# Optimization experiments

Hardware: AMD Instinct MI355X
Metric: run time of the kernel (lower is better)

The kernel has to match this reference:

```python
import jax, jax.numpy as jnp
import numpy as np
import math

E = 4096  # embed_dim
H = 32    # num_heads
M = 256   # max_queries
B = 8     # batch
N = 256   # kv tokens (16x16 grid -> no pos-embed interpolation branch)


def _sincos_1d(d, pos):
    omega = np.arange(d // 2, dtype=np.float32) / (d / 2.0)
    omega = 1.0 / 10000 ** omega
    out = np.einsum('m,d->md', pos.reshape(-1), omega)
    return np.concatenate([np.sin(out), np.cos(out)], axis=1)


def _sincos_2d(embed_dim, grid_size):
    gh = np.arange(grid_size, dtype=np.float32)
    gw = np.arange(grid_size, dtype=np.float32)
    grid = np.stack(np.meshgrid(gw, gh), axis=0).reshape(2, -1)
    return np.concatenate([
        _sincos_1d(embed_dim // 2, grid[0]),
        _sincos_1d(embed_dim // 2, grid[1]),
    ], axis=1)


def setup_inputs() -> dict:
    key = jax.random.key(0)
    ks = jax.random.split(key, 4)
    grid_size = int(math.ceil(math.sqrt(M)))
    pe = _sincos_2d(E, grid_size)[:M].astype(np.float32)
    return {
        'x': jax.random.normal(ks[0], (B, N, E), jnp.float32),
        'query': 0.02 * jax.random.normal(ks[1], (M, E), jnp.float32),
        'pos_embed': jnp.asarray(pe),
        'ln_q_w': jnp.ones((E,), jnp.float32),
        'ln_q_b': jnp.zeros((E,), jnp.float32),
        'ln_kv_w': jnp.ones((E,), jnp.float32),
        'ln_kv_b': jnp.zeros((E,), jnp.float32),
        'in_proj_w': 0.02 * jax.random.normal(ks[2], (3 * E, E), jnp.float32),
        'in_proj_b': jnp.zeros((3 * E,), jnp.float32),
        'out_proj_w': 0.02 * jax.random.normal(ks[3], (E, E), jnp.float32),
        'out_proj_b': jnp.zeros((E,), jnp.float32),
    }


def _ln(x, w, b, eps=1e-5):
    m = jnp.mean(x, -1, keepdims=True)
    v = jnp.mean((x - m) ** 2, -1, keepdims=True)
    return (x - m) * jax.lax.rsqrt(v + eps) * w + b


def reference(x, query, pos_embed, ln_q_w, ln_q_b, ln_kv_w, ln_kv_b,
              in_proj_w, in_proj_b, out_proj_w, out_proj_b):
    D = E // H
    kv = _ln(x, ln_kv_w, ln_kv_b)                      # [B,N,E] (kv_proj is Identity)
    q_in = _ln(query, ln_q_w, ln_q_b) + pos_embed      # [M,E] (Q + posQ, shared over batch)
    k_in = kv + pos_embed[None]                        # N == M so posK == pos_embed (no interp)
    Wq, Wk, Wv = in_proj_w[:E], in_proj_w[E:2 * E], in_proj_w[2 * E:]
    bq, bk, bv = in_proj_b[:E], in_proj_b[E:2 * E], in_proj_b[2 * E:]
    q = (q_in @ Wq.T + bq).reshape(M, H, D).transpose(1, 0, 2)          # [H,M,D]
    k = (k_in @ Wk.T + bk).reshape(B, N, H, D).transpose(0, 2, 1, 3)    # [B,H,N,D]
    v = (kv @ Wv.T + bv).reshape(B, N, H, D).transpose(0, 2, 1, 3)      # [B,H,N,D]
    scores = jnp.einsum('hmd,bhnd->bhmn', q, k) / jnp.sqrt(jnp.float32(D))
    attn = jax.nn.softmax(scores, axis=-1)                              # [B,H,M,N]
    o = jnp.einsum('bhmn,bhnd->bhmd', attn, v)
    o = o.transpose(0, 2, 1, 3).reshape(B, M, E)
    out = o @ out_proj_w.T + out_proj_b                                 # [B,M,E]
    # need_weights=True with average_attn_weights=True -> head-averaged weights
    return out, attn.mean(axis=1)
```

## Files before the change

kernel.cpp:

```cpp
#include <hip/hip_runtime.h>
#include <hip/hip_bf16.h>

typedef __bf16 bf16;
typedef __attribute__((ext_vector_type(8))) __bf16 bf16x8;
typedef __attribute__((ext_vector_type(4))) __bf16 bf16x4;
typedef __attribute__((ext_vector_type(4))) float floatx4;

#define E_DIM 4096
#define H_DIM 32
#define D_DIM 128
#define M_DIM 256
#define B_DIM 8
#define N_DIM 256

#define GLD_LDS(g, l) __builtin_amdgcn_global_load_lds( \
    (const __attribute__((address_space(1))) unsigned int*)(g), \
    (__attribute__((address_space(3))) unsigned int*)(l), 16, 0, 0)

__device__ __forceinline__ float wave_sum(float v) {
#pragma unroll
  for (int o = 32; o; o >>= 1) v += __shfl_xor(v, o);
  return v;
}
__device__ __forceinline__ float wave_max(float v) {
#pragma unroll
  for (int o = 32; o; o >>= 1) v = fmaxf(v, __shfl_xor(v, o));
  return v;
}

__global__ __launch_bounds__(256) void cvt_all_kernel(const float* __restrict__ s1,
                                                      bf16* __restrict__ d1,
                                                      const float* __restrict__ s2,
                                                      bf16* __restrict__ d2) {
  long i = ((long)blockIdx.x * 256 + threadIdx.x) * 8;
  const float* src;
  bf16* dst;
  if (i < 50331648L) { src = s1 + i; dst = d1 + i; }
  else { src = s2 + (i - 50331648L); dst = d2 + (i - 50331648L); }
  float4 a = *(const float4*)(src);
  float4 b = *(const float4*)(src + 4);
  bf16x8 p;
  p[0] = (bf16)a.x; p[1] = (bf16)a.y; p[2] = (bf16)a.z; p[3] = (bf16)a.w;
  p[4] = (bf16)b.x; p[5] = (bf16)b.y; p[6] = (bf16)b.z; p[7] = (bf16)b.w;
  *(bf16x8*)(dst) = p;
}

__global__ __launch_bounds__(256) void ln_x_kernel(const float* __restrict__ x,
                                                   const float* __restrict__ w,
                                                   const float* __restrict__ bvec,
                                                   const float* __restrict__ pos,
                                                   bf16* __restrict__ kv,
                                                   bf16* __restrict__ kin) {
  const int row = blockIdx.x;
  const int n = row & (N_DIM - 1);
  const int tid = threadIdx.x, wid = tid >> 6, lane = tid & 63;
  const float* xr = x + (size_t)row * E_DIM;
  float4 v[4];
  float s1 = 0.f, s2 = 0.f;
#pragma unroll
  for (int j = 0; j < 4; ++j) {
    v[j] = *(const float4*)(xr + j * 1024 + tid * 4);
    s1 += v[j].x + v[j].y + v[j].z + v[j].w;
    s2 += v[j].x * v[j].x + v[j].y * v[j].y + v[j].z * v[j].z + v[j].w * v[j].w;
  }
  s1 = wave_sum(s1); s2 = wave_sum(s2);
  __shared__ float red[8];
  if (lane == 0) { red[wid] = s1; red[wid + 4] = s2; }
  __syncthreads();
  s1 = red[0] + red[1] + red[2] + red[3];
  s2 = red[4] + red[5] + red[6] + red[7];
  const float mean = s1 * (1.f / E_DIM);
  const float var = s2 * (1.f / E_DIM) - mean * mean;
  const float rs = rsqrtf(var + 1e-5f);
#pragma unroll
  for (int j = 0; j < 4; ++j) {
    const int idx = j * 1024 + tid * 4;
    float4 wv = *(const float4*)(w + idx);
    float4 bv = *(const float4*)(bvec + idx);
    float4 pv = *(const float4*)(pos + (size_t)n * E_DIM + idx);
    float y0 = (v[j].x - mean) * rs * wv.x + bv.x;
    float y1 = (v[j].y - mean) * rs * wv.y + bv.y;
    float y2 = (v[j].z - mean) * rs * wv.z + bv.z;
    float y3 = (v[j].w - mean) * rs * wv.w + bv.w;
    bf16x4 a; a[0] = (bf16)y0; a[1] = (bf16)y1; a[2] = (bf16)y2; a[3] = (bf16)y3;
    *(bf16x4*)(kv + (size_t)row * E_DIM + idx) = a;
    bf16x4 c; c[0] = (bf16)(y0 + pv.x); c[1] = (bf16)(y1 + pv.y);
    c[2] = (bf16)(y2 + pv.z); c[3] = (bf16)(y3 + pv.w);
    *(bf16x4*)(kin + (size_t)row * E_DIM + idx) = c;
  }
}

__global__ __launch_bounds__(256) void ln_q_kernel(const float* __restrict__ q,
                                                   const float* __restrict__ w,
                                                   const float* __restrict__ bvec,
                                                   const float* __restrict__ pos,
                                                   bf16* __restrict__ qin) {
  const int row = blockIdx.x;
  const int tid = threadIdx.x, wid = tid >> 6, lane = tid & 63;
  const float* xr = q + (size_t)row * E_DIM;
  float4 v[4];
  float s1 = 0.f, s2 = 0.f;
#pragma unroll
  for (int j = 0; j < 4; ++j) {
    v[j] = *(const float4*)(xr + j * 1024 + tid * 4);
    s1 += v[j].x + v[j].y + v[j].z + v[j].w;
    s2 += v[j].x * v[j].x + v[j].y * v[j].y + v[j].z * v[j].z + v[j].w * v[j].w;
  }
  s1 = wave_sum(s1); s2 = wave_sum(s2);
  __shared__ float red[8];
  if (lane == 0) { red[wid] = s1; red[wid + 4] = s2; }
  __syncthreads();
  s1 = red[0] + red[1] + red[2] + red[3];
  s2 = red[4] + red[5] + red[6] + red[7];
  const float mean = s1 * (1.f / E_DIM);
  const float var = s2 * (1.f / E_DIM) - mean * mean;
  const float rs = rsqrtf(var + 1e-5f);
#pragma unroll
  for (int j = 0; j < 4; ++j) {
    const int idx = j * 1024 + tid * 4;
    float4 wv = *(const float4*)(w + idx);
    float4 bv = *(const float4*)(bvec + idx);
    float4 pv = *(const float4*)(pos + (size_t)row * E_DIM + idx);
    bf16x4 a;
    a[0] = (bf16)((v[j].x - mean) * rs * wv.x + bv.x + pv.x);
    a[1] = (bf16)((v[j].y - mean) * rs * wv.y + bv.y + pv.y);
    a[2] = (bf16)((v[j].z - mean) * rs * wv.z + bv.z + pv.z);
    a[3] = (bf16)((v[j].w - mean) * rs * wv.w + bv.w + pv.w);
    *(bf16x4*)(qin + (size_t)row * E_DIM + idx) = a;
  }
}

__global__ __launch_bounds__(256, 4)
void proj_fused(const bf16* __restrict__ qin, const bf16* __restrict__ kin,
                const bf16* __restrict__ kv, const bf16* __restrict__ Wqkv,
                const float* __restrict__ bqkv, bf16* __restrict__ qp,
                bf16* __restrict__ kp, bf16* __restrict__ vt) {
  __shared__ __align__(16) bf16 As[4096];
  __shared__ __align__(16) bf16 Bs[4096];
  const int tid = threadIdx.x;
  const int wid = tid >> 6;
  const int lane = tid & 63;

  const int id = blockIdx.x;
  int role, bx, by;
  const bf16 *A, *B;
  const float* bias;
  bf16* C;
  if (id < 512) {
    role = 1; bx = id & 31; by = id >> 5;
    A = kin; B = Wqkv + 16777216; bias = bqkv + 4096; C = kp;
  } else if (id < 1024) {
    role = 2; bx = (id - 512) & 31; by = (id - 512) >> 5;
    A = kv; B = Wqkv + 33554432; bias = bqkv + 8192; C = vt;
  } else {
    role = 0; bx = (id - 1024) & 31; by = (id - 1024) >> 5;
    A = qin; B = Wqkv; bias = bqkv; C = qp;
  }

  const bf16* Arow = A + (size_t)(by * 128) * E_DIM;
  const bf16* Brow = B + (size_t)(bx * 128) * E_DIM;

  const int s0 = wid * 2;
  const int srow = lane >> 2;
  const int skoff = (lane & 3) * 8;

  floatx4 acc[4][4];
#pragma unroll
  for (int i = 0; i < 4; ++i)
#pragma unroll
    for (int j = 0; j < 4; ++j) acc[i][j] = (floatx4){0.f, 0.f, 0.f, 0.f};

  const int rA = (wid >> 1) * 64 + (lane & 15);
  const int rB = (wid & 1) * 64 + (lane & 15);
  const int q16 = (lane >> 4) * 8;

  for (int kt = 0; kt < 128; ++kt) {
    const int k0 = kt << 5;
#pragma unroll
    for (int c = 0; c < 2; ++c) {
      const int s = s0 + c;
      const int row = s * 16 + srow;
      GLD_LDS(Arow + (size_t)row * E_DIM + k0 + skoff, As + s * 512);
      GLD_LDS(Brow + (size_t)row * E_DIM + k0 + skoff, Bs + s * 512);
    }
    asm volatile("s_waitcnt vmcnt(0)" ::: "memory");
    __syncthreads();

    bf16x8 af[4], bfr[4];
#pragma unroll
    for (int t = 0; t < 4; ++t) {
      af[t] = *(const bf16x8*)(As + (rA + t * 16) * 32 + q16);
      bfr[t] = *(const bf16x8*)(Bs + (rB + t * 16) * 32 + q16);
    }
#pragma unroll
    for (int tr = 0; tr < 4; ++tr)
#pragma unroll
      for (int tc = 0; tc < 4; ++tc)
        acc[tr][tc] = __builtin_amdgcn_mfma_f32_16x16x32_bf16(af[tr], bfr[tc],
                                                              acc[tr][tc], 0, 0, 0);
    __syncthreads();
  }

  const int mb = by * 128 + (wid >> 1) * 64 + (lane >> 4) * 4;
  const int nb = bx * 128 + (wid & 1) * 64 + (lane & 15);
#pragma unroll
  for (int tr = 0; tr < 4; ++tr) {
#pragma unroll
    for (int tc = 0; tc < 4; ++tc) {
      const int row0 = mb + tr * 16;
      const int col = nb + tc * 16;
      const float bb = bias[col];
      floatx4 a = acc[tr][tc];
      if (role != 2) {
#pragma unroll
        for (int r = 0; r < 4; ++r)
          C[(size_t)(row0 + r) * E_DIM + col] = (bf16)(a[r] + bb);
      } else {
        const int h = col >> 7, d = col & 127;
        const int b_ = row0 >> 8, n_ = row0 & 255;
        bf16x4 p;
#pragma unroll
        for (int r = 0; r < 4; ++r) p[r] = (bf16)(a[r] + bb);
        *(bf16x4*)(C + ((size_t)((b_ * H_DIM + h) * D_DIM + d)) * N_DIM + n_) = p;
      }
    }
  }
}

template <int MODE>
__global__ __launch_bounds__(256, 4)
void gemm_bt(const bf16* __restrict__ Abase, const bf16* __restrict__ Bbase,
             float* __restrict__ Cf, bf16* __restrict__ Cb,
             int K, int lda, int ldb, int ldc, float scale) {
  __shared__ __align__(16) bf16 As[4096];
  __shared__ __align__(16) bf16 Bs[4096];
  const int tid = threadIdx.x;
  const int wid = tid >> 6;
  const int lane = tid & 63;

  const bf16* A = Abase;
  const bf16* B = Bbase;
  int zb = 0, zh = 0;
  if constexpr (MODE == 2) {
    int z = blockIdx.z; zb = z >> 5; zh = z & 31;
    A += zh * D_DIM;
    B += ((size_t)zb * N_DIM) * E_DIM + zh * D_DIM;
  } else if constexpr (MODE == 3) {
    int z = blockIdx.z; zb = z >> 5; zh = z & 31;
    A += (size_t)z * M_DIM * 512;
    B += (size_t)z * D_DIM * N_DIM;
  } else if constexpr (MODE == 5) {
    A += blockIdx.z * 2048;
    B += blockIdx.z * 2048;
  }

  const bf16* Arow = A + (size_t)(blockIdx.y * 128) * lda;
  const bf16* Brow = B + (size_t)(blockIdx.x * 128) * ldb;

  const int s0 = wid * 2;
  const int srow = lane >> 2;
  const int skoff = (lane & 3) * 8;

  floatx4 acc[4][4];
#pragma unroll
  for (int i = 0; i < 4; ++i)
#pragma unroll
    for (int j = 0; j < 4; ++j) acc[i][j] = (floatx4){0.f, 0.f, 0.f, 0.f};

  const int rA = (wid >> 1) * 64 + (lane & 15);
  const int rB = (wid & 1) * 64 + (lane & 15);
  const int q16 = (lane >> 4) * 8;

  const int kTiles = K >> 5;
  for (int kt = 0; kt < kTiles; ++kt) {
    const int k0 = kt << 5;
#pragma unroll
    for (int c = 0; c < 2; ++c) {
      const int s = s0 + c;
      const int row = s * 16 + srow;
      GLD_LDS(Arow + (size_t)row * lda + k0 + skoff, As + s * 512);
      GLD_LDS(Brow + (size_t)row * ldb + k0 + skoff, Bs + s * 512);
    }
    asm volatile("s_waitcnt vmcnt(0)" ::: "memory");
    __syncthreads();

    bf16x8 af[4], bfr[4];
#pragma unroll
    for (int t = 0; t < 4; ++t) {
      af[t] = *(const bf16x8*)(As + (rA + t * 16) * 32 + q16);
      bfr[t] = *(const bf16x8*)(Bs + (rB + t * 16) * 32 + q16);
    }
#pragma unroll
    for (int tr = 0; tr < 4; ++tr)
#pragma unroll
      for (int tc = 0; tc < 4; ++tc)
        acc[tr][tc] = __builtin_amdgcn_mfma_f32_16x16x32_bf16(af[tr], bfr[tc],
                                                              acc[tr][tc], 0, 0, 0);
    __syncthreads();
  }

  const int mb = blockIdx.y * 128 + (wid >> 1) * 64 + (lane >> 4) * 4;
  const int nb = blockIdx.x * 128 + (wid & 1) * 64 + (lane & 15);
#pragma unroll
  for (int tr = 0; tr < 4; ++tr) {
#pragma unroll
    for (int tc = 0; tc < 4; ++tc) {
      const int row0 = mb + tr * 16;
      const int col = nb + tc * 16;
      floatx4 a = acc[tr][tc];
      if constexpr (MODE == 2) {
#pragma unroll
        for (int r = 0; r < 4; ++r)
          Cf[(size_t)blockIdx.z * (M_DIM * N_DIM) + (size_t)(row0 + r) * ldc + col] =
              a[r] * scale;
      } else if constexpr (MODE == 3) {
        int z = blockIdx.z; int zb_ = z >> 5, zh_ = z & 31;
#pragma unroll
        for (int r = 0; r < 4; ++r)
          Cb[(size_t)zb_ * M_DIM * E_DIM + (size_t)(row0 + r) * E_DIM + zh_ * D_DIM + col] =
              (bf16)a[r];
      } else {
#pragma unroll
        for (int r = 0; r < 4; ++r)
          Cf[(size_t)blockIdx.z * 8388608 + (size_t)(row0 + r) * ldc + col] = a[r];
      }
    }
  }
}

__global__ __launch_bounds__(256) void reduce_out_kernel(const float* __restrict__ p,
                                                         const float* __restrict__ bias,
                                                         float* __restrict__ out) {
  const size_t i = ((size_t)blockIdx.x * 256 + threadIdx.x) * 4;
  float4 a = *(const float4*)(p + i);
  float4 b = *(const float4*)(p + 8388608 + i);
  float4 bb = *(const float4*)(bias + (i & 4095));
  float4 o;
  o.x = a.x + b.x + bb.x; o.y = a.y + b.y + bb.y;
  o.z = a.z + b.z + bb.z; o.w = a.w + b.w + bb.w;
  *(float4*)(out + i) = o;
}

__global__ __launch_bounds__(256) void softmax_mean_kernel(float* __restrict__ scores,
                                                           float* __restrict__ out_mean) {
  const int bm = blockIdx.x;
  const int b = bm >> 8, m = bm & 255;
  const int wid = threadIdx.x >> 6, lane = threadIdx.x & 63;
  float a0 = 0.f, a1 = 0.f, a2 = 0.f, a3 = 0.f;
  for (int j = 0; j < 8; ++j) {
    const int h = wid * 8 + j;
    float* row = scores + ((size_t)((b * H_DIM + h) * M_DIM + m)) * N_DIM;
    float4 v = *(const float4*)(row + lane * 4);
    float mx = fmaxf(fmaxf(v.x, v.y), fmaxf(v.z, v.w));
    mx = wave_max(mx);
    v.x = __expf(v.x - mx); v.y = __expf(v.y - mx);
    v.z = __expf(v.z - mx); v.w = __expf(v.w - mx);
    const float s = wave_sum(v.x + v.y + v.z + v.w);
    const float inv = 1.f / s;
    v.x *= inv; v.y *= inv; v.z *= inv; v.w *= inv;
    a0 += v.x; a1 += v.y; a2 += v.z; a3 += v.w;
    bf16x4 p; p[0] = (bf16)v.x; p[1] = (bf16)v.y; p[2] = (bf16)v.z; p[3] = (bf16)v.w;
    *(bf16x4*)((bf16*)row + lane * 4) = p;
  }
  __shared__ float red[4][256];
  *(float4*)&red[wid][lane * 4] = make_float4(a0, a1, a2, a3);
  __syncthreads();
  if (wid == 0) {
    float4 r0 = *(float4*)&red[0][lane * 4];
    float4 r1 = *(float4*)&red[1][lane * 4];
    float4 r2 = *(float4*)&red[2][lane * 4];
    float4 r3 = *(float4*)&red[3][lane * 4];
    float4 o;
    o.x = (r0.x + r1.x + r2.x + r3.x) * (1.f / H_DIM);
    o.y = (r0.y + r1.y + r2.y + r3.y) * (1.f / H_DIM);
    o.z = (r0.z + r1.z + r2.z + r3.z) * (1.f / H_DIM);
    o.w = (r0.w + r1.w + r2.w + r3.w) * (1.f / H_DIM);
    *(float4*)(out_mean + (size_t)bm * N_DIM + lane * 4) = o;
  }
}

extern "C" void kernel_launch(void* const* d_in, const int* in_sizes, int n_in,
                              void* d_out, int out_size, void* d_ws, size_t ws_size,
                              hipStream_t stream) {
  const float* x = (const float*)d_in[0];
  const float* query = (const float*)d_in[1];
  const float* pos = (const float*)d_in[2];
  const float* ln_q_w = (const float*)d_in[3];
  const float* ln_q_b = (const float*)d_in[4];
  const float* ln_kv_w = (const float*)d_in[5];
  const float* ln_kv_b = (const float*)d_in[6];
  const float* Wqkv_f = (const float*)d_in[7];
  const float* bqkv = (const float*)d_in[8];
  const float* Wout_f = (const float*)d_in[9];
  const float* bout = (const float*)d_in[10];

  char* ws = (char*)d_ws;
  bf16* Wqkv = (bf16*)(ws + 0);
  bf16* Wout = (bf16*)(ws + 100663296);
  bf16* kv   = (bf16*)(ws + 134217728);
  bf16* kin  = (bf16*)(ws + 150994944);
  bf16* qin  = (bf16*)(ws + 167772160);
  bf16* qp   = (bf16*)(ws + 169869312);
  bf16* kp   = (bf16*)(ws + 171966464);
  bf16* vt   = (bf16*)(ws + 188743680);
  float* partials = (float*)(ws + 205520896);
  float* scores = (float*)(ws + 0);
  bf16* obuf = (bf16*)(ws + 67108864);

  float* out = (float*)d_out;
  float* out2 = out + (size_t)B_DIM * M_DIM * E_DIM;

  cvt_all_kernel<<<32768, 256, 0, stream>>>(Wqkv_f, Wqkv, Wout_f, Wout);
  ln_x_kernel<<<2048, 256, 0, stream>>>(x, ln_kv_w, ln_kv_b, pos, kv, kin);
  ln_q_kernel<<<256, 256, 0, stream>>>(query, ln_q_w, ln_q_b, pos, qin);

  proj_fused<<<1088, 256, 0, stream>>>(qin, kin, kv, Wqkv, bqkv, qp, kp, vt);

  gemm_bt<2><<<dim3(2, 2, 256), 256, 0, stream>>>(qp, kp, scores, nullptr,
                                                  128, 4096, 4096, 256,
                                                  0.08838834764831845f);
  softmax_mean_kernel<<<2048, 256, 0, stream>>>(scores, out2);
  gemm_bt<3><<<dim3(1, 2, 256), 256, 0, stream>>>((const bf16*)scores, vt,
                                                  nullptr, obuf,
                                                  256, 512, 256, 4096, 1.f);
  gemm_bt<5><<<dim3(32, 16, 2), 256, 0, stream>>>(obuf, Wout, partials, nullptr,
                                                  2048, 4096, 4096, 4096, 1.f);
  reduce_out_kernel<<<8192, 256, 0, stream>>>(partials, bout, out);
}
```

Baseline: 789.5 us.

## Double-buffer LDS tiles in shared GEMM core to overlap loads with MFMA

Moves the duplicated GEMM main loop from the projection kernel and the templated GEMM into one shared helper. The helper uses two LDS buffers for A and B, and prefetches the next K tile with global_load_lds while the MFMAs run on the current tile. This removes the explicit vmcnt(0) wait and one barrier per iteration, so global latency can be hidden behind compute. LDS per block doubles and launch bounds drop from 4 to 2 blocks per SM, which may lower occupancy. Correctness relies on the barrier making the async LDS loads visible.

```diff
diff --git a/kernel.cpp b/kernel.cpp
--- a/kernel.cpp
+++ b/kernel.cpp
@@ -26,6 +26,56 @@
 #pragma unroll
   for (int o = 32; o; o >>= 1) v = fmaxf(v, __shfl_xor(v, o));
   return v;
+}
+
+__device__ __forceinline__ void gemm_core(const bf16* __restrict__ Arow,
+                                          const bf16* __restrict__ Brow,
+                                          int lda, int ldb, int kTiles,
+                                          bf16* As, bf16* Bs,
+                                          floatx4 (&acc)[4][4],
+                                          int wid, int lane) {
+  const int s0 = wid * 2;
+  const int srow = lane >> 2;
+  const int skoff = (lane & 3) * 8;
+  const int rA = (wid >> 1) * 64 + (lane & 15);
+  const int rB = (wid & 1) * 64 + (lane & 15);
+  const int q16 = (lane >> 4) * 8;
+
+#pragma unroll
+  for (int c = 0; c < 2; ++c) {
+    const int s = s0 + c;
+    const int row = s * 16 + srow;
+    GLD_LDS(Arow + (size_t)row * lda + skoff, As + s * 512);
+    GLD_LDS(Brow + (size_t)row * ldb + skoff, Bs + s * 512);
+  }
+
+  for (int kt = 0; kt < kTiles; ++kt) {
+    const int cur = (kt & 1) * 4096;
+    const int nxt = 4096 - cur;
+    __syncthreads();
+    if (kt + 1 < kTiles) {
+      const int k0 = (kt + 1) << 5;
+#pragma unroll
+      for (int c = 0; c < 2; ++c) {
+        const int s = s0 + c;
+        const int row = s * 16 + srow;
+        GLD_LDS(Arow + (size_t)row * lda + k0 + skoff, As + nxt + s * 512);
+        GLD_LDS(Brow + (size_t)row * ldb + k0 + skoff, Bs + nxt + s * 512);
+      }
+    }
+    bf16x8 af[4], bfr[4];
+#pragma unroll
+    for (int t = 0; t < 4; ++t) {
+      af[t] = *(const bf16x8*)(As + cur + (rA + t * 16) * 32 + q16);
+      bfr[t] = *(const bf16x8*)(Bs + cur + (rB + t * 16) * 32 + q16);
+    }
+#pragma unroll
+    for (int tr = 0; tr < 4; ++tr)
+#pragma unroll
+      for (int tc = 0; tc < 4; ++tc)
+        acc[tr][tc] = __builtin_amdgcn_mfma_f32_16x16x32_bf16(af[tr], bfr[tc],
+                                                              acc[tr][tc], 0, 0, 0);
+  }
 }
 
 __global__ __launch_bounds__(256) void cvt_all_kernel(const float* __restrict__ s1,
@@ -130,13 +180,13 @@
   }
 }
 
-__global__ __launch_bounds__(256, 4)
+__global__ __launch_bounds__(256, 2)
 void proj_fused(const bf16* __restrict__ qin, const bf16* __restrict__ kin,
                 const bf16* __restrict__ kv, const bf16* __restrict__ Wqkv,
                 const float* __restrict__ bqkv, bf16* __restrict__ qp,
                 bf16* __restrict__ kp, bf16* __restrict__ vt) {
-  __shared__ __align__(16) bf16 As[4096];
-  __shared__ __align__(16) bf16 Bs[4096];
+  __shared__ __align__(16) bf16 As[8192];
+  __shared__ __align__(16) bf16 Bs[8192];
   const int tid = threadIdx.x;
   const int wid = tid >> 6;
   const int lane = tid & 63;
@@ -160,46 +210,13 @@
   const bf16* Arow = A + (size_t)(by * 128) * E_DIM;
   const bf16* Brow = B + (size_t)(bx * 128) * E_DIM;
 
-  const int s0 = wid * 2;
-  const int srow = lane >> 2;
-  const int skoff = (lane & 3) * 8;
-
   floatx4 acc[4][4];
 #pragma unroll
   for (int i = 0; i < 4; ++i)
 #pragma unroll
     for (int j = 0; j < 4; ++j) acc[i][j] = (floatx4){0.f, 0.f, 0.f, 0.f};
 
-  const int rA = (wid >> 1) * 64 + (lane & 15);
-  const int rB = (wid & 1) * 64 + (lane & 15);
-  const int q16 = (lane >> 4) * 8;
-
-  for (int kt = 0; kt < 128; ++kt) {
-    const int k0 = kt << 5;
-#pragma unroll
-    for (int c = 0; c < 2; ++c) {
-      const int s = s0 + c;
-      const int row = s * 16 + srow;
-      GLD_LDS(Arow + (size_t)row * E_DIM + k0 + skoff, As + s * 512);
-      GLD_LDS(Brow + (size_t)row * E_DIM + k0 + skoff, Bs + s * 512);
-    }
-    asm volatile("s_waitcnt vmcnt(0)" ::: "memory");
-    __syncthreads();
-
-    bf16x8 af[4], bfr[4];
-#pragma unroll
-    for (int t = 0; t < 4; ++t) {
-      af[t] = *(const bf16x8*)(As + (rA + t * 16) * 32 + q16);
-      bfr[t] = *(const bf16x8*)(Bs + (rB + t * 16) * 32 + q16);
-    }
-#pragma unroll
-    for (int tr = 0; tr < 4; ++tr)
-#pragma unroll
-      for (int tc = 0; tc < 4; ++tc)
-        acc[tr][tc] = __builtin_amdgcn_mfma_f32_16x16x32_bf16(af[tr], bfr[tc],
-                                                              acc[tr][tc], 0, 0, 0);
-    __syncthreads();
-  }
+  gemm_core(Arow, Brow, E_DIM, E_DIM, 128, As, Bs, acc, wid, lane);
 
   const int mb = by * 128 + (wid >> 1) * 64 + (lane >> 4) * 4;
   const int nb = bx * 128 + (wid & 1) * 64 + (lane & 15);
@@ -228,25 +245,24 @@
 }
 
 template <int MODE>
-__global__ __launch_bounds__(256, 4)
+__global__ __launch_bounds__(256, 2)
 void gemm_bt(const bf16* __restrict__ Abase, const bf16* __restrict__ Bbase,
              float* __restrict__ Cf, bf16* __restrict__ Cb,
              int K, int lda, int ldb, int ldc, float scale) {
-  __shared__ __align__(16) bf16 As[4096];
-  __shared__ __align__(16) bf16 Bs[4096];
+  __shared__ __align__(16) bf16 As[8192];
+  __shared__ __align__(16) bf16 Bs[8192];
   const int tid = threadIdx.x;
   const int wid = tid >> 6;
   const int lane = tid & 63;
 
   const bf16* A = Abase;
   const bf16* B = Bbase;
-  int zb = 0, zh = 0;
   if constexpr (MODE == 2) {
-    int z = blockIdx.z; zb = z >> 5; zh = z & 31;
+    int z = blockIdx.z; int zb = z >> 5, zh = z & 31;
     A += zh * D_DIM;
     B += ((size_t)zb * N_DIM) * E_DIM + zh * D_DIM;
   } else if constexpr (MODE == 3) {
-    int z = blockIdx.z; zb = z >> 5; zh = z & 31;
+    int z = blockIdx.z;
     A += (size_t)z * M_DIM * 512;
     B += (size_t)z * D_DIM * N_DIM;
   } else if constexpr (MODE == 5) {
@@ -257,47 +273,13 @@
   const bf16* Arow = A + (size_t)(blockIdx.y * 128) * lda;
   const bf16* Brow = B + (size_t)(blockIdx.x * 128) * ldb;
 
-  const int s0 = wid * 2;
-  const int srow = lane >> 2;
-  const int skoff = (lane & 3) * 8;
-
   floatx4 acc[4][4];
 #pragma unroll
   for (int i = 0; i < 4; ++i)
 #pragma unroll
     for (int j = 0; j < 4; ++j) acc[i][j] = (floatx4){0.f, 0.f, 0.f, 0.f};
 
-  const int rA = (wid >> 1) * 64 + (lane & 15);
-  const int rB = (wid & 1) * 64 + (lane & 15);
-  const int q16 = (lane >> 4) * 8;
-
-  const int kTiles = K >> 5;
-  for (int kt = 0; kt < kTiles; ++kt) {
-    const int k0 = kt << 5;
-#pragma unroll
-    for (int c = 0; c < 2; ++c) {
-      const int s = s0 + c;
-      const int row = s * 16 + srow;
-      GLD_LDS(Arow + (size_t)row * lda + k0 + skoff, As + s * 512);
-      GLD_LDS(Brow + (size_t)row * ldb + k0 + skoff, Bs + s * 512);
-    }
-    asm volatile("s_waitcnt vmcnt(0)" ::: "memory");
-    __syncthreads();
-
-    bf16x8 af[4], bfr[4];
-#pragma unroll
-    for (int t = 0; t < 4; ++t) {
-      af[t] = *(const bf16x8*)(As + (rA + t * 16) * 32 + q16);
-      bfr[t] = *(const bf16x8*)(Bs + (rB + t * 16) * 32 + q16);
-    }
-#pragma unroll
-    for (int tr = 0; tr < 4; ++tr)
-#pragma unroll
-      for (int tc = 0; tc < 4; ++tc)
-        acc[tr][tc] = __builtin_amdgcn_mfma_f32_16x16x32_bf16(af[tr], bfr[tc],
-                                                              acc[tr][tc], 0, 0, 0);
-    __syncthreads();
-  }
+  gemm_core(Arow, Brow, lda, ldb, K >> 5, As, Bs, acc, wid, lane);
 
   const int mb = blockIdx.y * 128 + (wid >> 1) * 64 + (lane >> 4) * 4;
   const int nb = blockIdx.x * 128 + (wid & 1) * 64 + (lane & 15);
```

Result: no change. 788.2 us (-0.2%).
